# Optimization experiments

Hardware: AMD Instinct MI355X
Metric: run time of the kernel (lower is better)

The kernel has to match this reference:

```python
import math
import jax, jax.numpy as jnp
import numpy as np

N_NODES = 200000          # len(tree)
HIDDEN = 1024             # args.hidden_dim
SINGLE_DIM = HIDDEN // 2  # lower/upper halves of the circle embedding
TREE_HEIGHT = 8           # path length (root-to-leaf)
BATCH = 2048              # positive pairs per step
N_NEG = 8                 # args.negative_sample_size
CIRCLE_MARGIN = 1.0       # args.circle_margin
SCR = 2.0 * math.pi       # single_circle_range


def setup_inputs() -> dict:
    key = jax.random.key(0)
    k1, k2, k3 = jax.random.split(key, 3)
    node_embedding = jax.random.normal(k1, (N_NODES, HIDDEN), dtype=jnp.float32)
    pos_path = jax.random.randint(k2, (BATCH, 2, TREE_HEIGHT), 0, N_NODES, dtype=jnp.int32)
    neg_path = jax.random.randint(k3, (BATCH, N_NEG, TREE_HEIGHT), 0, N_NODES, dtype=jnp.int32)
    return {"node_embedding": node_embedding, "pos_path": pos_path, "neg_path": neg_path}


def _inter_size(p1, p2):
    # |set(path1) & set(path2)| assuming distinct ids within a path.
    # p1: [..., P], p2: [..., P] -> [...]
    return (p1[..., :, None] == p2[..., None, :]).any(-1).sum(-1)


def _calc_dist(emb, p1, p2, diff):
    # emb: [V, H]; p1, p2: [..., P] int; diff: [...] float
    d = emb[p1] - emb[p2]                       # [..., P, H]
    low, high = d[..., :SINGLE_DIM], d[..., SINGLE_DIM:]
    dist = (0.5 * (low + high)).sum(-2)         # [..., SINGLE_DIM]
    return dist + (diff - 1.0)[..., None] * SCR


def reference(node_embedding, pos_path, neg_path):
    p1 = pos_path[:, 0]                          # [B, P]
    p2 = pos_path[:, 1]                          # [B, P]
    # calc_dist clamps diff to >= 1; calc_diff (used for k) does NOT.
    diff_pos = jnp.maximum(TREE_HEIGHT - _inter_size(p1, p2), 1).astype(jnp.float32)
    pos_dist = _calc_dist(node_embedding, p1, p2, diff_pos)          # [B, SD]

    diff_neg_raw = (TREE_HEIGHT - _inter_size(p1[:, None, :], neg_path)).astype(jnp.float32)  # [B, N]
    k = diff_neg_raw - 1.0                                            # unclamped, per source
    diff_neg = jnp.maximum(diff_neg_raw, 1.0)
    neg_dist = _calc_dist(node_embedding, p1[:, None, :], neg_path, diff_neg)  # [B, N, SD]

    tmp = k[..., None] * CIRCLE_MARGIN * SCR + pos_dist[:, None, :] - neg_dist  # [B, N, SD]
    tmp_p = jnp.maximum(tmp, 0.0)
    punish = jnp.sqrt((tmp_p * tmp_p).sum(-1)).sum()   # sum of per-(b,n) L2 norms
    return punish.reshape(1)
```

## Files before the change

kernel.cpp:

```cpp
#include <hip/hip_runtime.h>

constexpr int   TH    = 8;
constexpr int   NNEG  = 8;
constexpr int   HID4  = 256;
constexpr float SCR_F = 6.2831853071795864769f;

__global__ __launch_bounds__(64, 2)
void prep_kernel(const float* __restrict__ emb,
                 const int*   __restrict__ pos_path,
                 const int*   __restrict__ neg_path,
                 float*       __restrict__ sp2_out,
                 float*       __restrict__ C_out)
{
    const int b = blockIdx.x;
    const int l = threadIdx.x;

    if (l < NNEG) {
        int p1v[TH], p2v[TH];
#pragma unroll
        for (int i = 0; i < TH; i++) {
            p1v[i] = pos_path[b * 2 * TH + i];
            p2v[i] = pos_path[b * 2 * TH + TH + i];
        }
        int inter_pos = 0;
#pragma unroll
        for (int i = 0; i < TH; i++) {
            bool f = false;
#pragma unroll
            for (int j = 0; j < TH; j++) f = f || (p1v[i] == p2v[j]);
            inter_pos += f ? 1 : 0;
        }
        const float diff_pos = fmaxf((float)(TH - inter_pos), 1.0f);

        const int n = l;
        int negj[TH];
#pragma unroll
        for (int j = 0; j < TH; j++)
            negj[j] = neg_path[(b * NNEG + n) * TH + j];

        int inter_n = 0;
#pragma unroll
        for (int i = 0; i < TH; i++) {
            bool f = false;
#pragma unroll
            for (int j = 0; j < TH; j++) f = f || (p1v[i] == negj[j]);
            inter_n += f ? 1 : 0;
        }
        const int raw = TH - inter_n;
        C_out[b * NNEG + n] = (diff_pos - 1.0f - (raw == 0 ? 1.0f : 0.0f)) * SCR_F;
    }

    const float4* __restrict__ embv = (const float4*)emb;
    float4 s0 = {0.f, 0.f, 0.f, 0.f};
    float4 s1 = {0.f, 0.f, 0.f, 0.f};
#pragma unroll
    for (int h = 0; h < TH; h++) {
        const int r = pos_path[b * 2 * TH + TH + h];
        const float4* row = embv + (long)r * HID4;
        const float4 a0 = row[l];
        const float4 a1 = row[64 + l];
        const float4 a2 = row[128 + l];
        const float4 a3 = row[192 + l];
        s0.x += a0.x + a2.x; s0.y += a0.y + a2.y;
        s0.z += a0.z + a2.z; s0.w += a0.w + a2.w;
        s1.x += a1.x + a3.x; s1.y += a1.y + a3.y;
        s1.z += a1.z + a3.z; s1.w += a1.w + a3.w;
    }
    float4* sp2v = (float4*)sp2_out;
    sp2v[(long)b * 128 + l]      = s0;
    sp2v[(long)b * 128 + 64 + l] = s1;
}

__global__ __launch_bounds__(64, 2)
void neg_kernel(const float* __restrict__ emb,
                const int*   __restrict__ neg_path,
                const float* __restrict__ sp2_in,
                const float* __restrict__ C_in,
                float*       __restrict__ partial,
                int batch)
{
    const int bn = blockIdx.x;
    const int b  = bn % batch;
    const int n  = bn / batch;
    const int l  = threadIdx.x;
    const int idx = b * NNEG + n;

    const int4* __restrict__ npv = (const int4*)(neg_path + (long)idx * TH);
    const int4 nlo = npv[0];
    const int4 nhi = npv[1];
    const int ridx[TH] = {nlo.x, nlo.y, nlo.z, nlo.w, nhi.x, nhi.y, nhi.z, nhi.w};
    const float c = C_in[idx];

    const float4* __restrict__ embv = (const float4*)emb;
    float4 s0 = {0.f, 0.f, 0.f, 0.f};
    float4 s1 = {0.f, 0.f, 0.f, 0.f};
#pragma unroll
    for (int h = 0; h < TH; h++) {
        const float4* row = embv + (long)ridx[h] * HID4;
        const float4 a0 = row[l];
        const float4 a1 = row[64 + l];
        const float4 a2 = row[128 + l];
        const float4 a3 = row[192 + l];
        s0.x += a0.x + a2.x; s0.y += a0.y + a2.y;
        s0.z += a0.z + a2.z; s0.w += a0.w + a2.w;
        s1.x += a1.x + a3.x; s1.y += a1.y + a3.y;
        s1.z += a1.z + a3.z; s1.w += a1.w + a3.w;
    }

    const float4* sp2v = (const float4*)sp2_in;
    const float4 p0 = sp2v[(long)b * 128 + l];
    const float4 p1 = sp2v[(long)b * 128 + 64 + l];

    float v, a = 0.f;
    v = c + 0.5f * (s0.x - p0.x); v = fmaxf(v, 0.f); a += v * v;
    v = c + 0.5f * (s0.y - p0.y); v = fmaxf(v, 0.f); a += v * v;
    v = c + 0.5f * (s0.z - p0.z); v = fmaxf(v, 0.f); a += v * v;
    v = c + 0.5f * (s0.w - p0.w); v = fmaxf(v, 0.f); a += v * v;
    v = c + 0.5f * (s1.x - p1.x); v = fmaxf(v, 0.f); a += v * v;
    v = c + 0.5f * (s1.y - p1.y); v = fmaxf(v, 0.f); a += v * v;
    v = c + 0.5f * (s1.z - p1.z); v = fmaxf(v, 0.f); a += v * v;
    v = c + 0.5f * (s1.w - p1.w); v = fmaxf(v, 0.f); a += v * v;

#pragma unroll
    for (int off = 32; off > 0; off >>= 1) {
        a += __shfl_down(a, off, 64);
    }
    if (l == 0) partial[idx] = sqrtf(a);
}

__global__ __launch_bounds__(1024)
void reduce_kernel(const float* __restrict__ partial, int nval,
                   float* __restrict__ out)
{
    const int t = threadIdx.x;
    float s = 0.f;
    for (int i = t; i < nval; i += 1024) s += partial[i];

#pragma unroll
    for (int off = 32; off > 0; off >>= 1) {
        s += __shfl_down(s, off, 64);
    }
    __shared__ float s_red[16];
    const int lane = t & 63;
    const int wid  = t >> 6;
    if (lane == 0) s_red[wid] = s;
    __syncthreads();
    if (t == 0) {
        float tot = 0.f;
#pragma unroll
        for (int w = 0; w < 16; w++) tot += s_red[w];
        out[0] = tot;
    }
}

extern "C" void kernel_launch(void* const* d_in, const int* in_sizes, int n_in,
                              void* d_out, int out_size, void* d_ws, size_t ws_size,
                              hipStream_t stream) {
    const float* emb      = (const float*)d_in[0];
    const int*   pos_path = (const int*)d_in[1];
    const int*   neg_path = (const int*)d_in[2];
    float*       out      = (float*)d_out;

    const int BATCH = in_sizes[1] / (2 * TH);

    float* sp2     = (float*)d_ws;
    float* Cb      = sp2 + (size_t)BATCH * 512;
    float* partial = Cb  + (size_t)BATCH * NNEG;

    prep_kernel<<<BATCH, 64, 0, stream>>>(emb, pos_path, neg_path, sp2, Cb);
    neg_kernel<<<BATCH * NNEG, 64, 0, stream>>>(emb, neg_path, sp2, Cb,
                                                partial, BATCH);
    reduce_kernel<<<1, 1024, 0, stream>>>(partial, BATCH * NNEG, out);
}
```

Before: 973.9 us.

## Pre-fold referenced embedding rows into half-width table before gathering

Adds a pass that marks every node referenced by the positive or negative paths. For each marked row, a fold kernel writes low+high (512 floats) into a workspace table. The prep and neg kernels then gather 2KB folded rows instead of 4KB full rows, halving the bytes per gather and reading each unique row from HBM only once, in row order. In exchange it adds three kernel launches, a flag scatter, writes to a large workspace table, and depends on the workspace being big enough.

```diff
diff --git a/kernel.cpp b/kernel.cpp
--- a/kernel.cpp
+++ b/kernel.cpp
@@ -3,10 +3,67 @@
 constexpr int   TH    = 8;
 constexpr int   NNEG  = 8;
 constexpr int   HID4  = 256;
+constexpr int   FOLD4 = 128;
 constexpr float SCR_F = 6.2831853071795864769f;
 
+__global__ __launch_bounds__(256)
+void flag_zero(int* __restrict__ flags, int n)
+{
+    for (int i = blockIdx.x * 256 + threadIdx.x; i < n; i += gridDim.x * 256)
+        flags[i] = 0;
+}
+
+__global__ __launch_bounds__(256)
+void flag_set(const int* __restrict__ pos_path,
+              const int* __restrict__ neg_path,
+              int* __restrict__ flags, int batch)
+{
+    const int tid = blockIdx.x * 256 + threadIdx.x;
+    const int np2 = batch * TH;
+    const int tot = np2 + batch * NNEG * TH;
+    if (tid >= tot) return;
+    int r;
+    if (tid < np2) {
+        const int b = tid / TH, h = tid % TH;
+        r = pos_path[b * 2 * TH + TH + h];
+    } else {
+        r = neg_path[tid - np2];
+    }
+    flags[r] = 1;
+}
+
+__global__ __launch_bounds__(256)
+void fold_kernel(const float* __restrict__ emb,
+                 const int*   __restrict__ flags,
+                 float*       __restrict__ folded,
+                 int n_nodes)
+{
+    const int lane = threadIdx.x & 63;
+    const int wave = blockIdx.x * 4 + (threadIdx.x >> 6);
+    const int nwaves = gridDim.x * 4;
+
+    const float4* __restrict__ embv = (const float4*)emb;
+    float4* __restrict__ fv = (float4*)folded;
+
+    for (int r = wave; r < n_nodes; r += nwaves) {
+        if (!flags[r]) continue;
+        const float4* row = embv + (long)r * HID4;
+        const float4 a0 = row[lane];
+        const float4 a1 = row[64 + lane];
+        const float4 a2 = row[128 + lane];
+        const float4 a3 = row[192 + lane];
+        float4 o0, o1;
+        o0.x = a0.x + a2.x; o0.y = a0.y + a2.y;
+        o0.z = a0.z + a2.z; o0.w = a0.w + a2.w;
+        o1.x = a1.x + a3.x; o1.y = a1.y + a3.y;
+        o1.z = a1.z + a3.z; o1.w = a1.w + a3.w;
+        fv[(long)r * FOLD4 + lane]      = o0;
+        fv[(long)r * FOLD4 + 64 + lane] = o1;
+    }
+}
+
 __global__ __launch_bounds__(64, 2)
-void prep_kernel(const float* __restrict__ emb,
+void prep_kernel(const float* __restrict__ folded,
                  const int*   __restrict__ pos_path,
                  const int*   __restrict__ neg_path,
                  float*       __restrict__ sp2_out,
@@ -50,29 +107,25 @@
         C_out[b * NNEG + n] = (diff_pos - 1.0f - (raw == 0 ? 1.0f : 0.0f)) * SCR_F;
     }
 
-    const float4* __restrict__ embv = (const float4*)emb;
+    const float4* __restrict__ fv = (const float4*)folded;
     float4 s0 = {0.f, 0.f, 0.f, 0.f};
     float4 s1 = {0.f, 0.f, 0.f, 0.f};
 #pragma unroll
     for (int h = 0; h < TH; h++) {
         const int r = pos_path[b * 2 * TH + TH + h];
-        const float4* row = embv + (long)r * HID4;
-        const float4 a0 = row[l];
-        const float4 a1 = row[64 + l];
-        const float4 a2 = row[128 + l];
-        const float4 a3 = row[192 + l];
-        s0.x += a0.x + a2.x; s0.y += a0.y + a2.y;
-        s0.z += a0.z + a2.z; s0.w += a0.w + a2.w;
-        s1.x += a1.x + a3.x; s1.y += a1.y + a3.y;
-        s1.z += a1.z + a3.z; s1.w += a1.w + a3.w;
+        const float4* row = fv + (long)r * FOLD4;
+        const float4 f0 = row[l];
+        const float4 f1 = row[64 + l];
+        s0.x += f0.x; s0.y += f0.y; s0.z += f0.z; s0.w += f0.w;
+        s1.x += f1.x; s1.y += f1.y; s1.z += f1.z; s1.w += f1.w;
     }
     float4* sp2v = (float4*)sp2_out;
-    sp2v[(long)b * 128 + l]      = s0;
-    sp2v[(long)b * 128 + 64 + l] = s1;
+    sp2v[(long)b * FOLD4 + l]      = s0;
+    sp2v[(long)b * FOLD4 + 64 + l] = s1;
 }
 
 __global__ __launch_bounds__(64, 2)
-void neg_kernel(const float* __restrict__ emb,
+void neg_kernel(const float* __restrict__ folded,
                 const int*   __restrict__ neg_path,
                 const float* __restrict__ sp2_in,
                 const float* __restrict__ C_in,
@@ -91,25 +144,21 @@
     const int ridx[TH] = {nlo.x, nlo.y, nlo.z, nlo.w, nhi.x, nhi.y, nhi.z, nhi.w};
     const float c = C_in[idx];
 
-    const float4* __restrict__ embv = (const float4*)emb;
+    const float4* __restrict__ fv = (const float4*)folded;
     float4 s0 = {0.f, 0.f, 0.f, 0.f};
     float4 s1 = {0.f, 0.f, 0.f, 0.f};
 #pragma unroll
     for (int h = 0; h < TH; h++) {
-        const float4* row = embv + (long)ridx[h] * HID4;
-        const float4 a0 = row[l];
-        const float4 a1 = row[64 + l];
-        const float4 a2 = row[128 + l];
-        const float4 a3 = row[192 + l];
-        s0.x += a0.x + a2.x; s0.y += a0.y + a2.y;
-        s0.z += a0.z + a2.z; s0.w += a0.w + a2.w;
-        s1.x += a1.x + a3.x; s1.y += a1.y + a3.y;
-        s1.z += a1.z + a3.z; s1.w += a1.w + a3.w;
+        const float4* row = fv + (long)ridx[h] * FOLD4;
+        const float4 f0 = row[l];
+        const float4 f1 = row[64 + l];
+        s0.x += f0.x; s0.y += f0.y; s0.z += f0.z; s0.w += f0.w;
+        s1.x += f1.x; s1.y += f1.y; s1.z += f1.z; s1.w += f1.w;
     }
 
     const float4* sp2v = (const float4*)sp2_in;
-    const float4 p0 = sp2v[(long)b * 128 + l];
-    const float4 p1 = sp2v[(long)b * 128 + 64 + l];
+    const float4 p0 = sp2v[(long)b * FOLD4 + l];
+    const float4 p1 = sp2v[(long)b * FOLD4 + 64 + l];
 
     float v, a = 0.f;
     v = c + 0.5f * (s0.x - p0.x); v = fmaxf(v, 0.f); a += v * v;
@@ -161,14 +210,23 @@
     const int*   neg_path = (const int*)d_in[2];
     float*       out      = (float*)d_out;
 
-    const int BATCH = in_sizes[1] / (2 * TH);
-
-    float* sp2     = (float*)d_ws;
+    const int BATCH   = in_sizes[1] / (2 * TH);
+    const int N_NODES = in_sizes[0] / 1024;
+
+    float* folded  = (float*)d_ws;
+    int*   flags   = (int*)(folded + (size_t)N_NODES * 512);
+    float* sp2     = (float*)(flags + N_NODES);
     float* Cb      = sp2 + (size_t)BATCH * 512;
     float* partial = Cb  + (size_t)BATCH * NNEG;
 
-    prep_kernel<<<BATCH, 64, 0, stream>>>(emb, pos_path, neg_path, sp2, Cb);
-    neg_kernel<<<BATCH * NNEG, 64, 0, stream>>>(emb, neg_path, sp2, Cb,
+    const int refs = BATCH * (TH + NNEG * TH);
+
+    flag_zero<<<512, 256, 0, stream>>>(flags, N_NODES);
+    flag_set<<<(refs + 255) / 256, 256, 0, stream>>>(pos_path, neg_path,
+                                                     flags, BATCH);
+    fold_kernel<<<2048, 256, 0, stream>>>(emb, flags, folded, N_NODES);
+    prep_kernel<<<BATCH, 64, 0, stream>>>(folded, pos_path, neg_path, sp2, Cb);
+    neg_kernel<<<BATCH * NNEG, 64, 0, stream>>>(folded, neg_path, sp2, Cb,
                                                 partial, BATCH);
     reduce_kernel<<<1, 1024, 0, stream>>>(partial, BATCH * NNEG, out);
 }
```

Result: slower. 1.042 ms (+7.0%).
